# Kernel tuning notes

Measured on AMD Instinct MI355X. Metric: run time of the kernel, lower is better.

Reference implementation:

```python
import jax, jax.numpy as jnp
import numpy as np

D = 1024      # hidden_dim
E = 8         # num_experts
H = 4096      # expert_hidden_dim (= 4*D, module default)
K = 2         # top-k experts per token


def setup_inputs() -> dict:
    key = jax.random.key(0)
    ks = jax.random.split(key, 7)
    s = 1.0 / np.sqrt(D)
    sh = 1.0 / np.sqrt(H)
    return {
        "x": jax.random.normal(ks[0], (4, 1024, D), dtype=jnp.float32),
        "W1": jax.random.uniform(ks[1], (E, D, H), jnp.float32, -s, s),
        "b1": jax.random.uniform(ks[2], (E, H), jnp.float32, -s, s),
        "W2": jax.random.uniform(ks[3], (E, H, D), jnp.float32, -sh, sh),
        "b2": jax.random.uniform(ks[4], (E, D), jnp.float32, -sh, sh),
        "Wg": jax.random.uniform(ks[5], (D, E), jnp.float32, -s, s),
        "bg": jax.random.uniform(ks[6], (E,), jnp.float32, -s, s),
    }


def reference(x, W1, b1, W2, b2, Wg, bg):
    orig_shape = x.shape
    x2d = x.reshape(-1, D)                                    # [N, D]
    gate_scores = jax.nn.softmax(x2d @ Wg + bg, axis=-1)      # [N, E]
    topk_scores, topk_idx = jax.lax.top_k(gate_scores, K)     # [N, K]
    # Dense all-experts 2-layer MLP (dropout is identity in eval mode)
    h = jax.nn.gelu(jnp.einsum('nd,edh->neh', x2d, W1) + b1[None], approximate=False)  # [N, E, H]
    expert_out = jnp.einsum('neh,ehd->ned', h, W2) + b2[None]  # [N, E, D]
    # Gather top-k expert outputs and combine with gate weights
    topk_out = jnp.take_along_axis(expert_out, topk_idx[:, :, None], axis=1)  # [N, K, D]
    out = jnp.sum(topk_out * topk_scores[:, :, None], axis=1)  # [N, D]
    return out.reshape(orig_shape)
```

## Files before the change

kernel.cpp:

```cpp
#include <hip/hip_runtime.h>
#include <math.h>

#define DIM  1024
#define NEXP 8
#define HID  4096
#define TOPK 2

typedef __attribute__((ext_vector_type(8))) short bf16x8;
typedef __attribute__((ext_vector_type(4))) float f32x4;

__device__ inline unsigned short f2bf(float f) {
  union { float f; unsigned int u; } v; v.f = f;
  unsigned int u = v.u;
  return (unsigned short)((u + 0x7FFFu + ((u >> 16) & 1u)) >> 16);
}

__device__ inline void load_lds16(const void* g, void* l) {
  __builtin_amdgcn_global_load_lds(
      (const __attribute__((address_space(1))) void*)g,
      (__attribute__((address_space(3))) void*)l, 16, 0, 0);
}

__global__ void gate_kernel(const float* __restrict__ x,
                            const float* __restrict__ Wg,
                            const float* __restrict__ bg,
                            float* __restrict__ topk_score,
                            int* __restrict__ count,
                            int* __restrict__ lists,
                            int N) {
  int n = blockIdx.x;
  if (n >= N) return;
  int lane = threadIdx.x;
  float acc[NEXP];
#pragma unroll
  for (int e = 0; e < NEXP; ++e) acc[e] = 0.f;
  const float* xr = x + (size_t)n * DIM;
  for (int d = lane; d < DIM; d += 64) {
    float xv = xr[d];
    const float* w = Wg + (size_t)d * NEXP;
#pragma unroll
    for (int e = 0; e < NEXP; ++e) acc[e] += xv * w[e];
  }
#pragma unroll
  for (int off = 32; off > 0; off >>= 1) {
#pragma unroll
    for (int e = 0; e < NEXP; ++e) acc[e] += __shfl_xor(acc[e], off, 64);
  }
  if (lane == 0) {
    float l[NEXP];
#pragma unroll
    for (int e = 0; e < NEXP; ++e) l[e] = acc[e] + bg[e];
    float m = l[0];
#pragma unroll
    for (int e = 1; e < NEXP; ++e) m = fmaxf(m, l[e]);
    float p[NEXP];
    float s = 0.f;
#pragma unroll
    for (int e = 0; e < NEXP; ++e) { p[e] = expf(l[e] - m); s += p[e]; }
    int i0 = 0;
#pragma unroll
    for (int e = 1; e < NEXP; ++e) if (l[e] > l[i0]) i0 = e;
    int i1 = (i0 == 0) ? 1 : 0;
#pragma unroll
    for (int e = 0; e < NEXP; ++e) if (e != i0 && l[e] > l[i1]) i1 = e;
    float inv = 1.f / s;
    topk_score[n * TOPK + 0] = p[i0] * inv;
    topk_score[n * TOPK + 1] = p[i1] * inv;
    int pos0 = atomicAdd(&count[i0], 1);
    lists[(size_t)i0 * N + pos0] = n * TOPK + 0;
    int pos1 = atomicAdd(&count[i1], 1);
    lists[(size_t)i1 * N + pos1] = n * TOPK + 1;
  }
}

__global__ void offsets_kernel(const int* __restrict__ count, int* __restrict__ offsets,
                               int* __restrict__ tiles, int* __restrict__ ntiles) {
  if (threadIdx.x == 0 && blockIdx.x == 0) {
    int s = 0, nt = 0;
    for (int e = 0; e < NEXP; ++e) {
      offsets[e] = s;
      int c = count[e];
      s += c;
      int rts = (c + 255) >> 8;
      for (int i = 0; i < rts; ++i) tiles[nt++] = (e << 16) | i;
    }
    offsets[NEXP] = s;
    ntiles[0] = nt;
  }
}

__global__ void gather_kernel(const float* __restrict__ x,
                              const int* __restrict__ offsets,
                              const int* __restrict__ lists,
                              unsigned short* __restrict__ Xg,
                              int* __restrict__ pairmap,
                              int N) {
  int g = blockIdx.x;
  int e = 0;
  while (e < NEXP - 1 && g >= offsets[e + 1]) ++e;
  int i = g - offsets[e];
  int ent = lists[(size_t)e * N + i];
  int tok = ent >> 1;
  if (threadIdx.x == 0) pairmap[g] = ent;
  float4 v = *((const float4*)(x + (size_t)tok * DIM) + threadIdx.x);
  ushort4 o;
  o.x = f2bf(v.x); o.y = f2bf(v.y); o.z = f2bf(v.z); o.w = f2bf(v.w);
  *((ushort4*)(Xg + (size_t)g * DIM) + threadIdx.x) = o;
}

__global__ __launch_bounds__(256) void transpose_convert(
    const float* __restrict__ src, unsigned short* __restrict__ dst, int R, int C) {
  const int e = blockIdx.z;
  src += (size_t)e * R * C;
  dst += (size_t)e * R * C;
  const int r0 = blockIdx.x * 64, c0 = blockIdx.y * 64;
  __shared__ unsigned short Ts[64][68];
  const int t = threadIdx.x;
  const int rr = t >> 4, cc = (t & 15) * 4;
#pragma unroll
  for (int p = 0; p < 4; ++p) {
    int r = rr + p * 16;
    float4 v = *(const float4*)(src + (size_t)(r0 + r) * C + c0 + cc);
    Ts[cc + 0][r] = f2bf(v.x);
    Ts[cc + 1][r] = f2bf(v.y);
    Ts[cc + 2][r] = f2bf(v.z);
    Ts[cc + 3][r] = f2bf(v.w);
  }
  __syncthreads();
  const int cr = t >> 3, rq = (t & 7) * 8;
#pragma unroll
  for (int p = 0; p < 2; ++p) {
    int c = cr + p * 32;
    ushort4 a = *(ushort4*)&Ts[c][rq];
    ushort4 b = *(ushort4*)&Ts[c][rq + 4];
    *(ushort4*)(dst + (size_t)(c0 + c) * R + r0 + rq) = a;
    *(ushort4*)(dst + (size_t)(c0 + c) * R + r0 + rq + 4) = b;
  }
}

template <int PASS>
__global__ __launch_bounds__(512, 2) void moe_gemm8(
    const unsigned short* __restrict__ Asrc,
    const unsigned short* __restrict__ Bt,
    const float* __restrict__ bias,
    const int* __restrict__ offsets,
    const int* __restrict__ tiles,
    const int* __restrict__ ntiles,
    const int* __restrict__ pairmap,
    const float* __restrict__ score,
    unsigned short* __restrict__ Hmat,
    float* __restrict__ out,
    int maxt) {
  constexpr int K  = (PASS == 1) ? DIM : HID;
  constexpr int NS = (PASS == 1) ? HID : DIM;
  constexpr int KS = (PASS == 1) ? 1 : 2;
  constexpr int KL = K / KS;
  constexpr int NT = KL / 64;

  const unsigned orig = blockIdx.x;
  const unsigned nwg = gridDim.x;
  const unsigned q = nwg >> 3, r8 = nwg & 7;
  const unsigned xcd = orig & 7, p8 = orig >> 3;
  const unsigned id = (xcd < r8 ? xcd * (q + 1) : r8 * (q + 1) + (xcd - r8) * q) + p8;
  const int tt = (int)(id % (unsigned)maxt);
  const int ct = (int)(id / (unsigned)maxt);

  if (tt >= ntiles[0]) return;
  const int pk = tiles[tt];
  const int e  = pk >> 16;
  const int rt = pk & 0xffff;
  const int gbase = offsets[e];
  const int nc = offsets[e + 1] - gbase;
  const int rowsvalid = min(256, nc - rt * 256);
  const int kz = (PASS == 1) ? 0 : blockIdx.z;
  const int koff = kz * KL;

  __shared__ unsigned short As[3][16384];
  __shared__ unsigned short Bs[3][8192];

  const int tid  = threadIdx.x;
  const int lane = tid & 63;
  const int wid  = tid >> 6;
  const int wr = (wid >> 1) * 64;
  const int wc = (wid & 1) * 64;
  const int fr = lane & 15;
  const int fq = lane >> 4;

  f32x4 acc[4][4];
#pragma unroll
  for (int m = 0; m < 4; ++m)
#pragma unroll
    for (int n = 0; n < 4; ++n) acc[m][n] = (f32x4){0.f, 0.f, 0.f, 0.f};

  const unsigned short* Ab = Asrc + (size_t)(gbase + rt * 256) * K + koff;
  const unsigned short* Bb = Bt + (size_t)e * NS * K + (size_t)ct * 128 * K + koff;

  auto stage = [&](int b, int k0) {
#pragma unroll
    for (int i = 0; i < 4; ++i) {
      const int c = i * 512 + tid;
      const int row = c >> 3;
      const int swz = (c & 7) ^ (row & 7);
      load_lds16(Ab + (size_t)row * K + k0 + swz * 8, (char*)As[b] + c * 16);
    }
#pragma unroll
    for (int i = 0; i < 2; ++i) {
      const int c = i * 512 + tid;
      const int row = c >> 3;
      const int swz = (c & 7) ^ (row & 7);
      load_lds16(Bb + (size_t)row * K + k0 + swz * 8, (char*)Bs[b] + c * 16);
    }
  };

  stage(0, 0);
  stage(1, 64);

  for (int t = 0; t < NT; ++t) {
    if (t + 2 < NT) {
      stage((t + 2) % 3, (t + 2) * 64);
      asm volatile("s_waitcnt vmcnt(12)" ::: "memory");
    } else if (t + 2 == NT) {
      asm volatile("s_waitcnt vmcnt(6)" ::: "memory");
    } else {
      asm volatile("s_waitcnt vmcnt(0)" ::: "memory");
    }
    __builtin_amdgcn_s_barrier();

    const unsigned short* Ac = As[t % 3];
    const unsigned short* Bc = Bs[t % 3];
#pragma unroll
    for (int kk = 0; kk < 2; ++kk) {
      bf16x8 af[4], bf[4];
#pragma unroll
      for (int m = 0; m < 4; ++m) {
        const int row = wr + m * 16 + fr;
        const int u = (kk * 4 + fq) ^ (row & 7);
        af[m] = *(const bf16x8*)&Ac[row * 64 + u * 8];
      }
#pragma unroll
      for (int n = 0; n < 4; ++n) {
        const int row = wc + n * 16 + fr;
        const int u = (kk * 4 + fq) ^ (row & 7);
        bf[n] = *(const bf16x8*)&Bc[row * 64 + u * 8];
      }
      __builtin_amdgcn_s_setprio(1);
#pragma unroll
      for (int m = 0; m < 4; ++m)
#pragma unroll
        for (int n = 0; n < 4; ++n)
          acc[m][n] = __builtin_amdgcn_mfma_f32_16x16x32_bf16(af[m], bf[n], acc[m][n], 0, 0, 0);
      __builtin_amdgcn_s_setprio(0);
    }
    __builtin_amdgcn_s_barrier();
  }

  if (PASS == 1) {
#pragma unroll
    for (int n = 0; n < 4; ++n) {
      const int col = ct * 128 + wc + n * 16 + fr;
      const float b1v = bias[(size_t)e * NS + col];
#pragma unroll
      for (int m = 0; m < 4; ++m) {
#pragma unroll
        for (int r = 0; r < 4; ++r) {
          const int lrow = wr + m * 16 + fq * 4 + r;
          if (lrow < rowsvalid) {
            float v = acc[m][n][r] + b1v;
            v = 0.5f * v * (1.f + erff(v * 0.70710678118654752440f));
            Hmat[(size_t)(gbase + rt * 256 + lrow) * HID + col] = f2bf(v);
          }
        }
      }
    }
  } else {
    float b2v[4];
#pragma unroll
    for (int n = 0; n < 4; ++n)
      b2v[n] = (kz == 0) ? bias[(size_t)e * NS + ct * 128 + wc + n * 16 + fr] : 0.f;
#pragma unroll
    for (int m = 0; m < 4; ++m) {
#pragma unroll
      for (int r = 0; r < 4; ++r) {
        const int lrow = wr + m * 16 + fq * 4 + r;
        if (lrow < rowsvalid) {
          const int g = gbase + rt * 256 + lrow;
          const int ent = pairmap[g];
          const int tok = ent >> 1;
          const float s = score[ent];
#pragma unroll
          for (int n = 0; n < 4; ++n) {
            const int col = ct * 128 + wc + n * 16 + fr;
            atomicAdd(&out[(size_t)tok * DIM + col], s * (acc[m][n][r] + b2v[n]));
          }
        }
      }
    }
  }
}

template <int PASS>
__global__ __launch_bounds__(256) void moe_gemm(
    const unsigned short* __restrict__ Asrc,
    const float* __restrict__ Bsrc,
    const float* __restrict__ bias,
    const int* __restrict__ offsets,
    const int* __restrict__ pairmap,
    const float* __restrict__ score,
    unsigned short* __restrict__ Hmat,
    float* __restrict__ out) {
  constexpr int K  = (PASS == 1) ? DIM : HID;
  constexpr int NS = (PASS == 1) ? HID : DIM;
  const int e = blockIdx.z;
  const int gbase = offsets[e];
  const int nc = offsets[e + 1] - gbase;
  const int rt = blockIdx.x;
  if (rt * 128 >= nc) return;
  const int rowsvalid = min(128, nc - rt * 128);
  const int ct = blockIdx.y;
  __shared__ unsigned short As[128 * 40];
  __shared__ unsigned short Bs[128 * 40];
  const int tid  = threadIdx.x;
  const int lane = tid & 63;
  const int wid  = tid >> 6;
  const int wr = (wid >> 1) * 64;
  const int wc = (wid & 1) * 64;
  const int fr = lane & 15;
  const int fq = lane >> 4;
  f32x4 acc[4][4];
#pragma unroll
  for (int m = 0; m < 4; ++m)
#pragma unroll
    for (int n = 0; n < 4; ++n) acc[m][n] = (f32x4){0.f, 0.f, 0.f, 0.f};
  const int ar = tid >> 1;
  const int ak = (tid & 1) * 16;
  int arow = rt * 128 + ((ar < rowsvalid) ? ar : 0);
  const unsigned short* Aptr = Asrc + (size_t)(gbase + arow) * K + ak;
  const int bc = (tid & 31) * 4;
  const int bk = (tid >> 5) * 4;
  const float* Bptr = Bsrc + (size_t)e * K * NS + (size_t)bk * NS + ct * 128 + bc;
  for (int k0 = 0; k0 < K; k0 += 32) {
    uint4 av0 = *(const uint4*)(Aptr + k0);
    uint4 av1 = *(const uint4*)(Aptr + k0 + 8);
    const float* bp = Bptr + (size_t)k0 * NS;
    float4 w0 = *(const float4*)(bp);
    float4 w1 = *(const float4*)(bp + NS);
    float4 w2 = *(const float4*)(bp + 2 * NS);
    float4 w3 = *(const float4*)(bp + 3 * NS);
    __syncthreads();
    *(uint4*)&As[ar * 40 + ak]     = av0;
    *(uint4*)&As[ar * 40 + ak + 8] = av1;
    {
      uint2 pv;
      pv.x = (unsigned int)f2bf(w0.x) | ((unsigned int)f2bf(w1.x) << 16);
      pv.y = (unsigned int)f2bf(w2.x) | ((unsigned int)f2bf(w3.x) << 16);
      *(uint2*)&Bs[(bc + 0) * 40 + bk] = pv;
      pv.x = (unsigned int)f2bf(w0.y) | ((unsigned int)f2bf(w1.y) << 16);
      pv.y = (unsigned int)f2bf(w2.y) | ((unsigned int)f2bf(w3.y) << 16);
      *(uint2*)&Bs[(bc + 1) * 40 + bk] = pv;
      pv.x = (unsigned int)f2bf(w0.z) | ((unsigned int)f2bf(w1.z) << 16);
      pv.y = (unsigned int)f2bf(w2.z) | ((unsigned int)f2bf(w3.z) << 16);
      *(uint2*)&Bs[(bc + 2) * 40 + bk] = pv;
      pv.x = (unsigned int)f2bf(w0.w) | ((unsigned int)f2bf(w1.w) << 16);
      pv.y = (unsigned int)f2bf(w2.w) | ((unsigned int)f2bf(w3.w) << 16);
      *(uint2*)&Bs[(bc + 3) * 40 + bk] = pv;
    }
    __syncthreads();
    bf16x8 af[4], bfr[4];
#pragma unroll
    for (int m = 0; m < 4; ++m)
      af[m] = *(const bf16x8*)&As[(wr + m * 16 + fr) * 40 + fq * 8];
#pragma unroll
    for (int n = 0; n < 4; ++n)
      bfr[n] = *(const bf16x8*)&Bs[(wc + n * 16 + fr) * 40 + fq * 8];
#pragma unroll
    for (int m = 0; m < 4; ++m)
#pragma unroll
      for (int n = 0; n < 4; ++n)
        acc[m][n] = __builtin_amdgcn_mfma_f32_16x16x32_bf16(af[m], bfr[n], acc[m][n], 0, 0, 0);
  }
  if (PASS == 1) {
#pragma unroll
    for (int n = 0; n < 4; ++n) {
      int col = ct * 128 + wc + n * 16 + fr;
      float b1v = bias[(size_t)e * NS + col];
#pragma unroll
      for (int m = 0; m < 4; ++m) {
#pragma unroll
        for (int r = 0; r < 4; ++r) {
          int lrow = wr + m * 16 + fq * 4 + r;
          if (lrow < rowsvalid) {
            float v = acc[m][n][r] + b1v;
            v = 0.5f * v * (1.f + erff(v * 0.70710678118654752440f));
            Hmat[(size_t)(gbase + rt * 128 + lrow) * HID + col] = f2bf(v);
          }
        }
      }
    }
  } else {
    float b2v[4];
#pragma unroll
    for (int n = 0; n < 4; ++n)
      b2v[n] = bias[(size_t)e * NS + ct * 128 + wc + n * 16 + fr];
#pragma unroll
    for (int m = 0; m < 4; ++m) {
#pragma unroll
      for (int r = 0; r < 4; ++r) {
        int lrow = wr + m * 16 + fq * 4 + r;
        if (lrow < rowsvalid) {
          int g = gbase + rt * 128 + lrow;
          int ent = pairmap[g];
          int tok = ent >> 1;
          float s = score[ent];
#pragma unroll
          for (int n = 0; n < 4; ++n) {
            int col = ct * 128 + wc + n * 16 + fr;
            atomicAdd(&out[(size_t)tok * DIM + col], s * (acc[m][n][r] + b2v[n]));
          }
        }
      }
    }
  }
}

extern "C" void kernel_launch(void* const* d_in, const int* in_sizes, int n_in,
                              void* d_out, int out_size, void* d_ws, size_t ws_size,
                              hipStream_t stream) {
  const float* x  = (const float*)d_in[0];
  const float* W1 = (const float*)d_in[1];
  const float* b1 = (const float*)d_in[2];
  const float* W2 = (const float*)d_in[3];
  const float* b2 = (const float*)d_in[4];
  const float* Wg = (const float*)d_in[5];
  const float* bg = (const float*)d_in[6];
  float* out = (float*)d_out;
  const int N  = in_sizes[0] / DIM;
  const int NP = N * TOPK;
  const int MAXT = NP / 256 + NEXP;

  char* ws = (char*)d_ws;
  size_t off = 0;
  auto alloc = [&](size_t bytes) -> void* {
    void* p = ws + off;
    off = (off + bytes + 255) & ~(size_t)255;
    return p;
  };
  int*   count      = (int*)alloc(NEXP * sizeof(int));
  int*   offsets    = (int*)alloc((NEXP + 1) * sizeof(int));
  int*   tiles      = (int*)alloc((size_t)MAXT * sizeof(int));
  int*   ntiles     = (int*)alloc(sizeof(int));
  float* topk_score = (float*)alloc((size_t)NP * sizeof(float));
  int*   lists      = (int*)alloc((size_t)NEXP * N * sizeof(int));
  int*   pairmap    = (int*)alloc((size_t)NP * sizeof(int));
  unsigned short* Xg   = (unsigned short*)alloc((size_t)(NP + 256) * DIM * sizeof(unsigned short));
  unsigned short* Hmat = (unsigned short*)alloc((size_t)(NP + 256) * HID * sizeof(unsigned short));
  unsigned short* W1T = (unsigned short*)alloc((size_t)NEXP * DIM * HID * sizeof(unsigned short));
  unsigned short* W2T = (unsigned short*)alloc((size_t)NEXP * HID * DIM * sizeof(unsigned short));
  size_t need_full = off;

  hipMemsetAsync(count, 0, NEXP * sizeof(int), stream);
  gate_kernel<<<N, 64, 0, stream>>>(x, Wg, bg, topk_score, count, lists, N);
  offsets_kernel<<<1, 64, 0, stream>>>(count, offsets, tiles, ntiles);
  gather_kernel<<<NP, DIM / 4, 0, stream>>>(x, offsets, lists, Xg, pairmap, N);
  hipMemsetAsync(out, 0, (size_t)out_size * sizeof(float), stream);

  if (ws_size >= need_full) {
    dim3 tg1(DIM / 64, HID / 64, NEXP);
    transpose_convert<<<tg1, 256, 0, stream>>>(W1, W1T, DIM, HID);
    dim3 tg2(HID / 64, DIM / 64, NEXP);
    transpose_convert<<<tg2, 256, 0, stream>>>(W2, W2T, HID, DIM);

    dim3 g1((HID / 128) * MAXT, 1, 1);
    moe_gemm8<1><<<g1, 512, 0, stream>>>(Xg, W1T, b1, offsets, tiles, ntiles,
                                         pairmap, topk_score, Hmat, out, MAXT);
    dim3 g2((DIM / 128) * MAXT, 1, 2);
    moe_gemm8<2><<<g2, 512, 0, stream>>>(Hmat, W2T, b2, offsets, tiles, ntiles,
                                         pairmap, topk_score, Hmat, out, MAXT);
  } else {
    const int RT = (N + 127) / 128;
    dim3 g1(RT, HID / 128, NEXP);
    moe_gemm<1><<<g1, 256, 0, stream>>>(Xg, W1, b1, offsets, pairmap, topk_score, Hmat, out);
    dim3 g2(RT, DIM / 128, NEXP);
    moe_gemm<2><<<g2, 256, 0, stream>>>(Hmat, W2, b2, offsets, pairmap, topk_score, Hmat, out);
  }
}
```

Before: 596.7 us.

## Store activations and weights in K-blocked 64-wide tiles for contiguous GEMM staging

Changes the layout of the gathered activations, the hidden matrix and the transposed weights to a K-block-major form in which each 64-column K slice of all rows is contiguous. Each stage load in the grouped GEMMs then reads one contiguous chunk instead of rows strided by K, which should improve DRAM/L2 locality and reduce TLB pressure. The producer kernels (gather, transpose, pass-1 epilogue) are rewritten to emit this layout. The gather write and the pass-1 epilogue stores become more scattered across blocks.

```diff
diff --git a/kernel.cpp b/kernel.cpp
--- a/kernel.cpp
+++ b/kernel.cpp
@@ -89,12 +89,13 @@
   }
 }
 
+template <int TILED>
 __global__ void gather_kernel(const float* __restrict__ x,
                               const int* __restrict__ offsets,
                               const int* __restrict__ lists,
                               unsigned short* __restrict__ Xg,
                               int* __restrict__ pairmap,
-                              int N) {
+                              int N, int NPAD) {
   int g = blockIdx.x;
   int e = 0;
   while (e < NEXP - 1 && g >= offsets[e + 1]) ++e;
@@ -102,13 +103,18 @@
   int ent = lists[(size_t)e * N + i];
   int tok = ent >> 1;
   if (threadIdx.x == 0) pairmap[g] = ent;
-  float4 v = *((const float4*)(x + (size_t)tok * DIM) + threadIdx.x);
+  int d0 = threadIdx.x * 4;
+  float4 v = *((const float4*)(x + (size_t)tok * DIM + d0));
   ushort4 o;
   o.x = f2bf(v.x); o.y = f2bf(v.y); o.z = f2bf(v.z); o.w = f2bf(v.w);
-  *((ushort4*)(Xg + (size_t)g * DIM) + threadIdx.x) = o;
-}
-
-__global__ __launch_bounds__(256) void transpose_convert(
+  if (TILED) {
+    *(ushort4*)(Xg + ((size_t)(d0 >> 6) * NPAD + g) * 64 + (d0 & 63)) = o;
+  } else {
+    *(ushort4*)(Xg + (size_t)g * DIM + d0) = o;
+  }
+}
+
+__global__ __launch_bounds__(256) void transpose_convert_t(
     const float* __restrict__ src, unsigned short* __restrict__ dst, int R, int C) {
   const int e = blockIdx.z;
   src += (size_t)e * R * C;
@@ -128,18 +134,20 @@
   }
   __syncthreads();
   const int cr = t >> 3, rq = (t & 7) * 8;
+  const size_t kbbase = (size_t)(r0 >> 6) * C;
 #pragma unroll
   for (int p = 0; p < 2; ++p) {
     int c = cr + p * 32;
     ushort4 a = *(ushort4*)&Ts[c][rq];
     ushort4 b = *(ushort4*)&Ts[c][rq + 4];
-    *(ushort4*)(dst + (size_t)(c0 + c) * R + r0 + rq) = a;
-    *(ushort4*)(dst + (size_t)(c0 + c) * R + r0 + rq + 4) = b;
+    unsigned short* dp = dst + (kbbase + (c0 + c)) * 64 + rq;
+    *(ushort4*)(dp) = a;
+    *(ushort4*)(dp + 4) = b;
   }
 }
 
 template <int PASS>
-__global__ __launch_bounds__(512, 2) void moe_gemm8(
+__global__ __launch_bounds__(512, 2) void moe_gemm9(
     const unsigned short* __restrict__ Asrc,
     const unsigned short* __restrict__ Bt,
     const float* __restrict__ bias,
@@ -150,12 +158,13 @@
     const float* __restrict__ score,
     unsigned short* __restrict__ Hmat,
     float* __restrict__ out,
-    int maxt) {
+    int maxt, int NPAD) {
   constexpr int K  = (PASS == 1) ? DIM : HID;
   constexpr int NS = (PASS == 1) ? HID : DIM;
   constexpr int KS = (PASS == 1) ? 1 : 2;
   constexpr int KL = K / KS;
   constexpr int NT = KL / 64;
+  constexpr int KBK = K / 64;
 
   const unsigned orig = blockIdx.x;
   const unsigned nwg = gridDim.x;
@@ -173,7 +182,7 @@
   const int nc = offsets[e + 1] - gbase;
   const int rowsvalid = min(256, nc - rt * 256);
   const int kz = (PASS == 1) ? 0 : blockIdx.z;
-  const int koff = kz * KL;
+  const int kb0 = (kz * KL) >> 6;
 
   __shared__ unsigned short As[3][16384];
   __shared__ unsigned short Bs[3][8192];
@@ -192,32 +201,32 @@
 #pragma unroll
     for (int n = 0; n < 4; ++n) acc[m][n] = (f32x4){0.f, 0.f, 0.f, 0.f};
 
-  const unsigned short* Ab = Asrc + (size_t)(gbase + rt * 256) * K + koff;
-  const unsigned short* Bb = Bt + (size_t)e * NS * K + (size_t)ct * 128 * K + koff;
-
-  auto stage = [&](int b, int k0) {
+  const unsigned short* Ab = Asrc + ((size_t)kb0 * NPAD + (gbase + rt * 256)) * 64;
+  const unsigned short* Bb = Bt + (((size_t)e * KBK + kb0) * NS + (size_t)ct * 128) * 64;
+
+  auto stage = [&](int b, int t) {
+    const unsigned short* ga = Ab + (size_t)t * ((size_t)NPAD * 64);
+    const unsigned short* gb = Bb + (size_t)t * ((size_t)NS * 64);
 #pragma unroll
     for (int i = 0; i < 4; ++i) {
       const int c = i * 512 + tid;
-      const int row = c >> 3;
-      const int swz = (c & 7) ^ (row & 7);
-      load_lds16(Ab + (size_t)row * K + k0 + swz * 8, (char*)As[b] + c * 16);
+      const int off = ((c >> 3) * 8 + ((c & 7) ^ ((c >> 3) & 7))) * 8;
+      load_lds16(ga + off, (char*)As[b] + c * 16);
     }
 #pragma unroll
     for (int i = 0; i < 2; ++i) {
       const int c = i * 512 + tid;
-      const int row = c >> 3;
-      const int swz = (c & 7) ^ (row & 7);
-      load_lds16(Bb + (size_t)row * K + k0 + swz * 8, (char*)Bs[b] + c * 16);
+      const int off = ((c >> 3) * 8 + ((c & 7) ^ ((c >> 3) & 7))) * 8;
+      load_lds16(gb + off, (char*)Bs[b] + c * 16);
     }
   };
 
   stage(0, 0);
-  stage(1, 64);
+  stage(1, 1);
 
   for (int t = 0; t < NT; ++t) {
     if (t + 2 < NT) {
-      stage((t + 2) % 3, (t + 2) * 64);
+      stage((t + 2) % 3, t + 2);
       asm volatile("s_waitcnt vmcnt(12)" ::: "memory");
     } else if (t + 2 == NT) {
       asm volatile("s_waitcnt vmcnt(6)" ::: "memory");
@@ -255,9 +264,11 @@
   }
 
   if (PASS == 1) {
+    const size_t cb = (size_t)(ct * 2 + (wc >> 6));
 #pragma unroll
     for (int n = 0; n < 4; ++n) {
       const int col = ct * 128 + wc + n * 16 + fr;
+      const int cl = n * 16 + fr;
       const float b1v = bias[(size_t)e * NS + col];
 #pragma unroll
       for (int m = 0; m < 4; ++m) {
@@ -267,7 +278,7 @@
           if (lrow < rowsvalid) {
             float v = acc[m][n][r] + b1v;
             v = 0.5f * v * (1.f + erff(v * 0.70710678118654752440f));
-            Hmat[(size_t)(gbase + rt * 256 + lrow) * HID + col] = f2bf(v);
+            Hmat[(cb * NPAD + (gbase + rt * 256 + lrow)) * 64 + cl] = f2bf(v);
           }
         }
       }
@@ -435,6 +446,7 @@
   float* out = (float*)d_out;
   const int N  = in_sizes[0] / DIM;
   const int NP = N * TOPK;
+  const int NPAD = NP + 256;
   const int MAXT = NP / 256 + NEXP;
 
   char* ws = (char*)d_ws;
@@ -451,8 +463,8 @@
   float* topk_score = (float*)alloc((size_t)NP * sizeof(float));
   int*   lists      = (int*)alloc((size_t)NEXP * N * sizeof(int));
   int*   pairmap    = (int*)alloc((size_t)NP * sizeof(int));
-  unsigned short* Xg   = (unsigned short*)alloc((size_t)(NP + 256) * DIM * sizeof(unsigned short));
-  unsigned short* Hmat = (unsigned short*)alloc((size_t)(NP + 256) * HID * sizeof(unsigned short));
+  unsigned short* Xg   = (unsigned short*)alloc((size_t)NPAD * DIM * sizeof(unsigned short));
+  unsigned short* Hmat = (unsigned short*)alloc((size_t)NPAD * HID * sizeof(unsigned short));
   unsigned short* W1T = (unsigned short*)alloc((size_t)NEXP * DIM * HID * sizeof(unsigned short));
   unsigned short* W2T = (unsigned short*)alloc((size_t)NEXP * HID * DIM * sizeof(unsigned short));
   size_t need_full = off;
@@ -460,22 +472,23 @@
   hipMemsetAsync(count, 0, NEXP * sizeof(int), stream);
   gate_kernel<<<N, 64, 0, stream>>>(x, Wg, bg, topk_score, count, lists, N);
   offsets_kernel<<<1, 64, 0, stream>>>(count, offsets, tiles, ntiles);
-  gather_kernel<<<NP, DIM / 4, 0, stream>>>(x, offsets, lists, Xg, pairmap, N);
   hipMemsetAsync(out, 0, (size_t)out_size * sizeof(float), stream);
 
   if (ws_size >= need_full) {
+    gather_kernel<1><<<NP, DIM / 4, 0, stream>>>(x, offsets, lists, Xg, pairmap, N, NPAD);
     dim3 tg1(DIM / 64, HID / 64, NEXP);
-    transpose_convert<<<tg1, 256, 0, stream>>>(W1, W1T, DIM, HID);
+    transpose_convert_t<<<tg1, 256, 0, stream>>>(W1, W1T, DIM, HID);
     dim3 tg2(HID / 64, DIM / 64, NEXP);
-    transpose_convert<<<tg2, 256, 0, stream>>>(W2, W2T, HID, DIM);
+    transpose_convert_t<<<tg2, 256, 0, stream>>>(W2, W2T, HID, DIM);
 
     dim3 g1((HID / 128) * MAXT, 1, 1);
-    moe_gemm8<1><<<g1, 512, 0, stream>>>(Xg, W1T, b1, offsets, tiles, ntiles,
-                                         pairmap, topk_score, Hmat, out, MAXT);
+    moe_gemm9<1><<<g1, 512, 0, stream>>>(Xg, W1T, b1, offsets, tiles, ntiles,
+                                         pairmap, topk_score, Hmat, out, MAXT, NPAD);
     dim3 g2((DIM / 128) * MAXT, 1, 2);
-    moe_gemm8<2><<<g2, 512, 0, stream>>>(Hmat, W2T, b2, offsets, tiles, ntiles,
-                                         pairmap, topk_score, Hmat, out, MAXT);
+    moe_gemm9<2><<<g2, 512, 0, stream>>>(Hmat, W2T, b2, offsets, tiles, ntiles,
+                                         pairmap, topk_score, Hmat, out, MAXT, NPAD);
   } else {
+    gather_kernel<0><<<NP, DIM / 4, 0, stream>>>(x, offsets, lists, Xg, pairmap, N, NPAD);
     const int RT = (N + 127) / 128;
     dim3 g1(RT, HID / 128, NEXP);
     moe_gemm<1><<<g1, 256, 0, stream>>>(Xg, W1, b1, offsets, pairmap, topk_score, Hmat, out);
```

After: 593.3 us. About the same (-0.6%).
